# Kernel tuning notes

Hardware: AMD Instinct MI355X
Metric: run time of the kernel (lower is better)

## Reference

```python
import jax, jax.numpy as jnp
import numpy as np

D_IN = 1024
D_OUT = 1024
NUM_HEADS = 16
HEAD_DIM = D_OUT // NUM_HEADS


def setup_inputs() -> dict:
    key = jax.random.key(0)
    kx, kq, kk, kv = jax.random.split(key, 4)
    x = jax.random.normal(kx, (2, 2048, D_IN), dtype=jnp.float32)
    W_q = jax.random.normal(kq, (D_IN, D_OUT), dtype=jnp.float32)
    W_k = jax.random.normal(kk, (D_IN, D_OUT), dtype=jnp.float32)
    W_v = jax.random.normal(kv, (D_IN, D_OUT), dtype=jnp.float32)
    return {"x": x, "W_q": W_q, "W_k": W_k, "W_v": W_v}


def reference(x, W_q, W_k, W_v):
    B, S, _ = x.shape
    H, Dh = NUM_HEADS, HEAD_DIM
    # project and split heads -> [B, H, S, Dh]
    q = (x @ W_q).reshape(B, S, H, Dh).transpose(0, 2, 1, 3)
    k = (x @ W_k).reshape(B, S, H, Dh).transpose(0, 2, 1, 3)
    v = (x @ W_v).reshape(B, S, H, Dh).transpose(0, 2, 1, 3)
    scores = jnp.einsum('bhqd,bhkd->bhqk', q, k) / jnp.sqrt(jnp.float32(Dh))
    causal = jnp.tril(jnp.ones((S, S), dtype=bool))  # True where allowed
    scores = jnp.where(causal[None, None], scores, -jnp.inf)
    weights = jax.nn.softmax(scores, axis=-1)
    ctx = jnp.einsum('bhqk,bhkd->bhqd', weights, v)
    return ctx.transpose(0, 2, 1, 3).reshape(B, S, H * Dh)
```

## Files before the change

kernel.cpp:

```cpp
#include <hip/hip_runtime.h>
#include <hip/hip_bf16.h>

#define B 2
#define S 2048
#define DIN 1024
#define DOUT 1024
#define NH 16
#define DH 64
#define M_TOT (B * S)

typedef __attribute__((ext_vector_type(8))) short bf16x8;
typedef __attribute__((ext_vector_type(8))) unsigned short u16x8;
typedef __attribute__((ext_vector_type(4))) float f32x4;
typedef __attribute__((ext_vector_type(16))) float f32x16;

#define ASTRIDE 4194304
#define WSTRIDE 1048576

__device__ __forceinline__ ushort f2bf(float x) {
    union { float f; unsigned u; } c; c.f = x;
    unsigned r = (c.u + 0x7FFFu + ((c.u >> 16) & 1u)) >> 16;
    return (ushort)r;
}
__device__ __forceinline__ float bf2f(ushort h) {
    union { unsigned u; float f; } c; c.u = ((unsigned)h) << 16;
    return c.f;
}
__device__ __forceinline__ f32x4 mfma16(bf16x8 a, bf16x8 b, f32x4 c) {
    return __builtin_amdgcn_mfma_f32_16x16x32_bf16(a, b, c, 0, 0, 0);
}
__device__ __forceinline__ f32x16 mfma32(bf16x8 a, bf16x8 b, f32x16 c) {
    return __builtin_amdgcn_mfma_f32_32x32x16_bf16(a, b, c, 0, 0, 0);
}
__device__ __forceinline__ unsigned cvt_pk(float lo, float hi) {
    unsigned r;
    asm("v_cvt_pk_bf16_f32 %0, %1, %2" : "=v"(r) : "v"(lo), "v"(hi));
    return r;
}
__device__ __forceinline__ float exp2fast(float x) {
    float r;
    asm("v_exp_f32 %0, %1" : "=v"(r) : "v"(x));
    return r;
}


__global__ __launch_bounds__(256) void split_x(const float* __restrict__ x,
                                               ushort* __restrict__ xs) {
    const size_t gid = (size_t)blockIdx.x * 256 + threadIdx.x;
    const float4 v = *reinterpret_cast<const float4*>(x + gid * 4);
    const float in[4] = {v.x, v.y, v.z, v.w};
    ushort h0[4], h1[4];
#pragma unroll
    for (int e = 0; e < 4; ++e) {
        h0[e] = f2bf(in[e]);
        h1[e] = f2bf(in[e] - bf2f(h0[e]));
    }
    const size_t o = gid * 4;
    *reinterpret_cast<ushort4*>(xs + o)           = ushort4{h0[0], h0[1], h0[2], h0[3]};
    *reinterpret_cast<ushort4*>(xs + ASTRIDE + o) = ushort4{h1[0], h1[1], h1[2], h1[3]};
}

__global__ __launch_bounds__(256) void split_wT3(const float* __restrict__ W0,
                                                 const float* __restrict__ W1,
                                                 const float* __restrict__ W2,
                                                 ushort* __restrict__ wt) {
    __shared__ float Ws[64][68];
    const int tid = threadIdx.x;
    const int k0 = blockIdx.x << 6;
    const int n0 = blockIdx.y << 6;
    const int wi = blockIdx.z;
    const float* W = (wi == 0) ? W0 : (wi == 1) ? W1 : W2;
    ushort* wto = wt + (size_t)wi * 2 * WSTRIDE;

    const int r = tid >> 2;
    const int cb = (tid & 3) << 2;
#pragma unroll
    for (int it = 0; it < 4; ++it) {
        const int c = cb + (it << 4);
        *reinterpret_cast<float4*>(&Ws[r][c]) =
            *reinterpret_cast<const float4*>(&W[(size_t)(k0 + r) * 1024 + n0 + c]);
    }
    __syncthreads();
    const int rn = tid >> 2;
    const int kc = (tid & 3) << 4;
    u16x8 o0[2], o1[2];
#pragma unroll
    for (int half = 0; half < 2; ++half)
#pragma unroll
        for (int i = 0; i < 8; ++i) {
            const float x = Ws[kc + (half << 3) + i][rn];
            const ushort a = f2bf(x);
            o0[half][i] = a;
            o1[half][i] = f2bf(x - bf2f(a));
        }
    const size_t base = (size_t)(n0 + rn) * 1024 + k0 + kc;
    *reinterpret_cast<u16x8*>(wto + base)               = o0[0];
    *reinterpret_cast<u16x8*>(wto + base + 8)           = o0[1];
    *reinterpret_cast<u16x8*>(wto + WSTRIDE + base)     = o1[0];
    *reinterpret_cast<u16x8*>(wto + WSTRIDE + base + 8) = o1[1];
}

__global__ __launch_bounds__(256, 2) void proj_fused5(const ushort* __restrict__ xsp,
                                                      const ushort* __restrict__ wtsp,
                                                      float* __restrict__ qf,
                                                      ushort* __restrict__ ksp,
                                                      ushort* __restrict__ vtsp) {
    __shared__ __align__(16) ushort SL[36864];

    const int tid = threadIdx.x;
    const int lane = tid & 63;
    const int w = tid >> 6;
    const int swz = (blockIdx.x & 7) * 64 + (blockIdx.x >> 3);
    const int n0 = (swz & 15) << 6;
    const int m0 = (swz >> 4) << 7;
    const int col = lane & 15;
    const int glane = lane >> 4;
    const int lrow = lane >> 3;
    const int sl8 = ((lane & 7) ^ lrow) << 3;

    f32x4 accq[2][4], acck[2][4], accv[2][4];
#pragma unroll
    for (int mi = 0; mi < 2; ++mi)
#pragma unroll
        for (int nj = 0; nj < 4; ++nj) {
            accq[mi][nj] = f32x4{0.f, 0.f, 0.f, 0.f};
            acck[mi][nj] = f32x4{0.f, 0.f, 0.f, 0.f};
            accv[mi][nj] = f32x4{0.f, 0.f, 0.f, 0.f};
        }

    for (int k0 = 0; k0 < DIN; k0 += 64) {
        __syncthreads();
#pragma unroll
        for (int i = 0; i < 18; ++i) {
            const int u = (i << 2) | w;
            const ushort* g;
            if (u < 32) {
                const int sp = u >> 4, rb = u & 15;
                g = xsp + (size_t)sp * ASTRIDE + (size_t)(m0 + (rb << 3) + lrow) * 1024 + k0 + sl8;
            } else {
                const int v = u - 32;
                const int bi = v >> 3;
                const int rb = v & 7;
                g = wtsp + (size_t)bi * WSTRIDE + (size_t)(n0 + (rb << 3) + lrow) * 1024 + k0 + sl8;
            }
            __builtin_amdgcn_global_load_lds(g, &SL[u * 512], 16, 0, 0);
        }
        __syncthreads();

#pragma unroll
        for (int st = 0; st < 2; ++st) {
            const int sw = (((st << 2) | glane) ^ (col & 7)) << 3;
            bf16x8 a[2][2];
#pragma unroll
            for (int sp = 0; sp < 2; ++sp)
#pragma unroll
                for (int mi = 0; mi < 2; ++mi) {
                    const int arow = (w << 5) + (mi << 4) + col;
                    a[sp][mi] = *reinterpret_cast<const bf16x8*>(&SL[sp * 8192 + arow * 64 + sw]);
                }
#pragma unroll
            for (int nj = 0; nj < 4; ++nj) {
                const int brow = (nj << 4) + col;
                const int bb = 16384 + brow * 64 + sw;
                const bf16x8 bq0 = *reinterpret_cast<const bf16x8*>(&SL[bb]);
                const bf16x8 bq1 = *reinterpret_cast<const bf16x8*>(&SL[bb + 4096]);
                const bf16x8 bk0 = *reinterpret_cast<const bf16x8*>(&SL[bb + 8192]);
                const bf16x8 bk1 = *reinterpret_cast<const bf16x8*>(&SL[bb + 12288]);
                const bf16x8 bv0 = *reinterpret_cast<const bf16x8*>(&SL[bb + 16384]);
#pragma unroll
                for (int mi = 0; mi < 2; ++mi) {
                    accq[mi][nj] = mfma16(a[0][mi], bq0, accq[mi][nj]);
                    accq[mi][nj] = mfma16(a[1][mi], bq0, accq[mi][nj]);
                    accq[mi][nj] = mfma16(a[0][mi], bq1, accq[mi][nj]);
                    acck[mi][nj] = mfma16(a[0][mi], bk0, acck[mi][nj]);
                    acck[mi][nj] = mfma16(a[1][mi], bk0, acck[mi][nj]);
                    acck[mi][nj] = mfma16(a[0][mi], bk1, acck[mi][nj]);
                    accv[mi][nj] = mfma16(bv0, a[0][mi], accv[mi][nj]);
                    accv[mi][nj] = mfma16(bv0, a[1][mi], accv[mi][nj]);
                }
            }
        }
    }

    const int b = m0 >> 11;
    const int h = n0 >> 6;
    const size_t bh_off = (size_t)(b * NH + h) * S * DH;
#pragma unroll
    for (int mi = 0; mi < 2; ++mi)
#pragma unroll
        for (int r = 0; r < 4; ++r) {
            const int srow = (m0 & (S - 1)) + (w << 5) + (mi << 4) + (glane << 2) + r;
#pragma unroll
            for (int nj = 0; nj < 4; ++nj) {
                const size_t o = bh_off + (size_t)srow * DH + (nj << 4) + col;
                qf[o] = accq[mi][nj][r];
                const float xk = acck[mi][nj][r];
                const ushort k0s = f2bf(xk);
                ksp[o] = k0s;
                ksp[ASTRIDE + o] = f2bf(xk - bf2f(k0s));
            }
        }

    const int cm = col >> 2;
    const int colp = (col & 3) | ((((cm & 1) << 1) | (cm >> 1)) << 2);
    const size_t vbh = (size_t)(b * NH + h) * DH * S;
#pragma unroll
    for (int mi = 0; mi < 2; ++mi) {
        const int s = (m0 & (S - 1)) + (w << 5) + (mi << 4) + colp;
#pragma unroll
        for (int nj = 0; nj < 4; ++nj)
#pragma unroll
            for (int r = 0; r < 4; ++r) {
                const int d = (nj << 4) + (glane << 2) + r;
                vtsp[vbh + (size_t)d * S + s] = f2bf(accv[mi][nj][r]);
            }
    }
}

__global__ __launch_bounds__(256, 2) void attn_mfma7(const float* __restrict__ Qf,
                                                     const ushort* __restrict__ ksp,
                                                     const ushort* __restrict__ vtsp,
                                                     float* __restrict__ out) {
    __shared__ __align__(16) ushort SB[2][12288];

    const int tid = threadIdx.x;
    const int lane = tid & 63;
    const int w = tid >> 6;

    const int xcd = blockIdx.x & 7;
    const int u_ = blockIdx.x >> 3;
    int bh, qt;
    if (u_ < 32) { bh = (xcd << 2) | (u_ >> 4);                 qt = 15 - (u_ & 15); }
    else         { const int v2 = u_ - 32; bh = (xcd << 2) | 2 | (v2 >> 4); qt = v2 & 15; }

    const int q0 = qt << 7;
    const int qw0 = q0 + (w << 5);
    const int hi = lane >> 5;
    const int ql = lane & 31;
    const int qg = qw0 + ql;
    const int lrow = lane >> 3;
    const int sl8 = ((lane & 7) ^ lrow) << 3;

    bf16x8 qb[3][4];
    {
        const float* qp = Qf + ((size_t)bh * S + qg) * DH + (hi << 3);
#pragma unroll
        for (int dc = 0; dc < 4; ++dc) {
            const float4 f0 = *reinterpret_cast<const float4*>(qp + (dc << 4));
            const float4 f1 = *reinterpret_cast<const float4*>(qp + (dc << 4) + 4);
            const float xs[8] = {f0.x, f0.y, f0.z, f0.w, f1.x, f1.y, f1.z, f1.w};
#pragma unroll
            for (int e = 0; e < 8; ++e) {
                const float x = xs[e] * 0.18033688011112042f;
                const ushort h0 = f2bf(x);
                const float r1 = x - bf2f(h0);
                const ushort h1 = f2bf(r1);
                qb[0][dc][e] = (short)h0;
                qb[1][dc][e] = (short)h1;
                qb[2][dc][e] = (short)f2bf(r1 - bf2f(h1));
            }
        }
    }

    f32x16 O[2];
#pragma unroll
    for (int ds = 0; ds < 2; ++ds)
#pragma unroll
        for (int r = 0; r < 16; ++r) O[ds][r] = 0.f;
    float m_ = -INFINITY, l_ = 0.f;

    const size_t kbase = (size_t)bh * S * DH;
    const size_t vbase = (size_t)bh * DH * S;

#define ISSUE_KV(K0, BUF)                                                               \
    {                                                                                   \
        _Pragma("unroll")                                                               \
        for (int i = 0; i < 6; ++i) {                                                   \
            const int u = (i << 2) | w;                                                 \
            const ushort* gp;                                                           \
            if (u < 16) {                                                               \
                const int sp = u >> 3, rb = u & 7;                                      \
                gp = ksp + (size_t)sp * ASTRIDE + kbase +                               \
                     (size_t)((K0) + (rb << 3) + lrow) * DH + sl8;                      \
            } else {                                                                    \
                const int rb = u & 7;                                                   \
                gp = vtsp + vbase + (size_t)((rb << 3) + lrow) * S + (K0) + sl8;        \
            }                                                                           \
            __builtin_amdgcn_global_load_lds(gp, &SB[BUF][u * 512], 16, 0, 0);          \
        }                                                                               \
    }

    ISSUE_KV(0, 0);
    __syncthreads();

    const int ktmax = (q0 >> 6) + 1;
    for (int kt = 0; kt <= ktmax; ++kt) {
        const int k0 = kt << 6;
        const int cur = kt & 1;
        if (kt < ktmax) ISSUE_KV(k0 + 64, cur ^ 1);

        const bool active = (k0 <= qw0 + 31);
        if (active) {
            const ushort* KL = &SB[cur][0];
            const ushort* VL = &SB[cur][8192];

            f32x16 Sf[2];
#pragma unroll
            for (int ks = 0; ks < 2; ++ks)
#pragma unroll
                for (int r = 0; r < 16; ++r) Sf[ks][r] = 0.f;
#pragma unroll
            for (int ks = 0; ks < 2; ++ks) {
#pragma unroll
                for (int dc = 0; dc < 4; ++dc) {
                    const int row = (ks << 5) + ql;
                    const int eo = row * 64 + ((((dc << 1) | hi) ^ (row & 7)) << 3);
                    const bf16x8 ka = *reinterpret_cast<const bf16x8*>(&KL[eo]);
                    const bf16x8 kb = *reinterpret_cast<const bf16x8*>(&KL[4096 + eo]);
                    Sf[ks] = mfma32(ka, qb[0][dc], Sf[ks]);
                    Sf[ks] = mfma32(ka, qb[1][dc], Sf[ks]);
                    Sf[ks] = mfma32(ka, qb[2][dc], Sf[ks]);
                    Sf[ks] = mfma32(kb, qb[0][dc], Sf[ks]);
                    Sf[ks] = mfma32(kb, qb[1][dc], Sf[ks]);
                }
            }

            if (k0 + 63 > qw0) {
#pragma unroll
                for (int ks = 0; ks < 2; ++ks)
#pragma unroll
                    for (int r = 0; r < 16; ++r) {
                        const int kg = k0 + (ks << 5) + (r & 3) + ((r >> 2) << 3) + (hi << 2);
                        if (kg > qg) Sf[ks][r] = -1e30f;
                    }
            }

            float mx[8];
#pragma unroll
            for (int i = 0; i < 8; ++i)
                mx[i] = fmaxf(fmaxf(Sf[0][i], Sf[0][i + 8]),
                              fmaxf(Sf[1][i], Sf[1][i + 8]));
            float rm = fmaxf(fmaxf(fmaxf(mx[0], mx[1]), fmaxf(mx[2], mx[3])),
                             fmaxf(fmaxf(mx[4], mx[5]), fmaxf(mx[6], mx[7])));
            rm = fmaxf(rm, __shfl_xor(rm, 32));
            if (__any(rm > m_ + 8.f)) {
                const float nm = fmaxf(m_, rm);
                const float sc = exp2fast(m_ - nm);
                m_ = nm;
                l_ *= sc;
#pragma unroll
                for (int ds = 0; ds < 2; ++ds)
#pragma unroll
                    for (int r = 0; r < 16; ++r) O[ds][r] *= sc;
            }

            float rsa[4] = {0.f, 0.f, 0.f, 0.f};
            bf16x8 pb[4];
#pragma unroll
            for (int ks = 0; ks < 2; ++ks) {
                float p[16];
#pragma unroll
                for (int r = 0; r < 16; ++r) {
                    p[r] = exp2fast(Sf[ks][r] - m_);
                    rsa[r & 3] += p[r];
                }
#pragma unroll
                for (int c = 0; c < 2; ++c) {
                    union { unsigned u[4]; bf16x8 v; } pw;
                    pw.u[0] = cvt_pk(p[(c << 3) + 0], p[(c << 3) + 1]);
                    pw.u[1] = cvt_pk(p[(c << 3) + 2], p[(c << 3) + 3]);
                    pw.u[2] = cvt_pk(p[(c << 3) + 4], p[(c << 3) + 5]);
                    pw.u[3] = cvt_pk(p[(c << 3) + 6], p[(c << 3) + 7]);
                    pb[(ks << 1) + c] = pw.v;
                }
            }
            float rs = (rsa[0] + rsa[1]) + (rsa[2] + rsa[3]);
            rs += __shfl_xor(rs, 32);
            l_ += rs;

#pragma unroll
            for (int ds = 0; ds < 2; ++ds)
#pragma unroll
                for (int kc = 0; kc < 4; ++kc) {
                    const int row = (ds << 5) + ql;
                    const int eo = row * 64 + ((((kc << 1) | hi) ^ (row & 7)) << 3);
                    const bf16x8 va = *reinterpret_cast<const bf16x8*>(&VL[eo]);
                    O[ds] = mfma32(va, pb[kc], O[ds]);
                }
        }
        __syncthreads();
    }

    const float inv = 1.f / l_;
    const int b = bh >> 4, h = bh & (NH - 1);
    float* op = out + ((size_t)(b * S + qg)) * DOUT + h * DH;
#pragma unroll
    for (int ds = 0; ds < 2; ++ds)
#pragma unroll
        for (int rg = 0; rg < 4; ++rg) {
            float4 v;
            v.x = O[ds][(rg << 2) + 0] * inv;
            v.y = O[ds][(rg << 2) + 1] * inv;
            v.z = O[ds][(rg << 2) + 2] * inv;
            v.w = O[ds][(rg << 2) + 3] * inv;
            *reinterpret_cast<float4*>(&op[(ds << 5) + (rg << 3) + (hi << 2)]) = v;
        }
#undef ISSUE_KV
}

__global__ __launch_bounds__(256) void proj_f32(const float* __restrict__ A,
                                                const float* __restrict__ W,
                                                float* __restrict__ outf) {
    __shared__ float As[16][68];
    __shared__ float Bs[16][68];
    const int tid = threadIdx.x;
    const int m0 = blockIdx.x * 64;
    const int n0 = blockIdx.y * 64;
    const int tm = tid >> 4, tn = tid & 15;
    const int la_r = tid >> 2, la_c = (tid & 3) << 2;
    const int lb_r = tid >> 4, lb_c = (tid & 15) << 2;

    float acc[4][4];
#pragma unroll
    for (int i = 0; i < 4; ++i)
#pragma unroll
        for (int j = 0; j < 4; ++j) acc[i][j] = 0.f;

    for (int k0 = 0; k0 < DIN; k0 += 16) {
        const float4 av = *reinterpret_cast<const float4*>(&A[(size_t)(m0 + la_r) * DIN + k0 + la_c]);
        const float4 bv = *reinterpret_cast<const float4*>(&W[(size_t)(k0 + lb_r) * DOUT + n0 + lb_c]);
        __syncthreads();
        As[la_c + 0][la_r] = av.x; As[la_c + 1][la_r] = av.y;
        As[la_c + 2][la_r] = av.z; As[la_c + 3][la_r] = av.w;
        *reinterpret_cast<float4*>(&Bs[lb_r][lb_c]) = bv;
        __syncthreads();
#pragma unroll
        for (int kk = 0; kk < 16; ++kk) {
            const float4 a = *reinterpret_cast<const float4*>(&As[kk][tm << 2]);
            const float4 b = *reinterpret_cast<const float4*>(&Bs[kk][tn << 2]);
            const float aa[4] = {a.x, a.y, a.z, a.w};
            const float bb[4] = {b.x, b.y, b.z, b.w};
#pragma unroll
            for (int i = 0; i < 4; ++i)
#pragma unroll
                for (int j = 0; j < 4; ++j) acc[i][j] += aa[i] * bb[j];
        }
    }
    const int b = m0 >> 11;
    const int s_base = (m0 & (S - 1)) + (tm << 2);
    const int h = n0 >> 6;
    const int dh = tn << 2;
    float* obase = outf + ((size_t)(b * NH + h) * S) * DH;
#pragma unroll
    for (int i = 0; i < 4; ++i) {
        float4 v;
        v.x = acc[i][0]; v.y = acc[i][1]; v.z = acc[i][2]; v.w = acc[i][3];
        *reinterpret_cast<float4*>(&obase[(size_t)(s_base + i) * DH + dh]) = v;
    }
}

__global__ __launch_bounds__(256) void attn_f32(const float* __restrict__ Q,
                                                const float* __restrict__ K,
                                                const float* __restrict__ V,
                                                float* __restrict__ out) {
    __shared__ float Qs[64][68];
    __shared__ float Ks[64][68];
    __shared__ float Vs[64][68];
    __shared__ float Ps[64][68];
    const int tid = threadIdx.x;
    const int bh = blockIdx.x & 31;
    const int qt = 31 - (blockIdx.x >> 5);
    const int q0 = qt << 6;
    const int tq = tid >> 4, tk = tid & 15;
    const int sr = tid >> 2, sc = (tid & 3) << 2;

    const float* qbase = Q + ((size_t)bh * S + q0) * DH;
    const float* kbase = K + (size_t)bh * S * DH;
    const float* vbase = V + (size_t)bh * S * DH;
#pragma unroll
    for (int it = 0; it < 4; ++it) {
        const int d0 = sc + (it << 4);
        const float4 v = *reinterpret_cast<const float4*>(&qbase[(size_t)sr * DH + d0]);
        Qs[d0 + 0][sr] = v.x; Qs[d0 + 1][sr] = v.y;
        Qs[d0 + 2][sr] = v.z; Qs[d0 + 3][sr] = v.w;
    }
    float C[4][4];
#pragma unroll
    for (int i = 0; i < 4; ++i)
#pragma unroll
        for (int j = 0; j < 4; ++j) C[i][j] = 0.f;
    float m[4] = {-1e30f, -1e30f, -1e30f, -1e30f};
    float l[4] = {0.f, 0.f, 0.f, 0.f};

    for (int kt = 0; kt <= qt; ++kt) {
        const int k0 = kt << 6;
        float4 kv[4], vv[4];
#pragma unroll
        for (int it = 0; it < 4; ++it) {
            const int d0 = sc + (it << 4);
            kv[it] = *reinterpret_cast<const float4*>(&kbase[(size_t)(k0 + sr) * DH + d0]);
            vv[it] = *reinterpret_cast<const float4*>(&vbase[(size_t)(k0 + sr) * DH + d0]);
        }
        __syncthreads();
#pragma unroll
        for (int it = 0; it < 4; ++it) {
            const int d0 = sc + (it << 4);
            Ks[d0 + 0][sr] = kv[it].x; Ks[d0 + 1][sr] = kv[it].y;
            Ks[d0 + 2][sr] = kv[it].z; Ks[d0 + 3][sr] = kv[it].w;
            *reinterpret_cast<float4*>(&Vs[sr][d0]) = vv[it];
        }
        __syncthreads();

        float s[4][4];
#pragma unroll
        for (int i = 0; i < 4; ++i)
#pragma unroll
            for (int j = 0; j < 4; ++j) s[i][j] = 0.f;
#pragma unroll 16
        for (int d = 0; d < 64; ++d) {
            const float4 qf4 = *reinterpret_cast<const float4*>(&Qs[d][tq << 2]);
            const float4 kf4 = *reinterpret_cast<const float4*>(&Ks[d][tk << 2]);
            const float qa[4] = {qf4.x, qf4.y, qf4.z, qf4.w};
            const float ka[4] = {kf4.x, kf4.y, kf4.z, kf4.w};
#pragma unroll
            for (int i = 0; i < 4; ++i)
#pragma unroll
                for (int j = 0; j < 4; ++j) s[i][j] += qa[i] * ka[j];
        }
        if (kt == qt) {
#pragma unroll
            for (int i = 0; i < 4; ++i) {
                const int qg = q0 + (tq << 2) + i;
#pragma unroll
                for (int j = 0; j < 4; ++j) {
                    const int kg = k0 + (tk << 2) + j;
                    s[i][j] = (kg <= qg) ? s[i][j] * 0.125f : -1e30f;
                }
            }
        } else {
#pragma unroll
            for (int i = 0; i < 4; ++i)
#pragma unroll
                for (int j = 0; j < 4; ++j) s[i][j] *= 0.125f;
        }
#pragma unroll
        for (int i = 0; i < 4; ++i) {
            float rm = fmaxf(fmaxf(s[i][0], s[i][1]), fmaxf(s[i][2], s[i][3]));
#pragma unroll
            for (int off = 1; off < 16; off <<= 1) rm = fmaxf(rm, __shfl_xor(rm, off));
            const float mn = fmaxf(m[i], rm);
            const float scale = __expf(m[i] - mn);
            float rs = 0.f;
#pragma unroll
            for (int j = 0; j < 4; ++j) {
                s[i][j] = __expf(s[i][j] - mn);
                rs += s[i][j];
            }
#pragma unroll
            for (int off = 1; off < 16; off <<= 1) rs += __shfl_xor(rs, off);
            l[i] = l[i] * scale + rs;
            m[i] = mn;
#pragma unroll
            for (int j = 0; j < 4; ++j) C[i][j] *= scale;
            *reinterpret_cast<float4*>(&Ps[(tq << 2) + i][tk << 2]) =
                make_float4(s[i][0], s[i][1], s[i][2], s[i][3]);
        }
        __syncthreads();
#pragma unroll 4
        for (int kc = 0; kc < 16; ++kc) {
            float4 pf[4], vf[4];
#pragma unroll
            for (int i = 0; i < 4; ++i)
                pf[i] = *reinterpret_cast<const float4*>(&Ps[(tq << 2) + i][kc << 2]);
#pragma unroll
            for (int j = 0; j < 4; ++j)
                vf[j] = *reinterpret_cast<const float4*>(&Vs[(kc << 2) + j][tk << 2]);
#pragma unroll
            for (int i = 0; i < 4; ++i) {
                const float pa[4] = {pf[i].x, pf[i].y, pf[i].z, pf[i].w};
#pragma unroll
                for (int j = 0; j < 4; ++j) {
                    C[i][j] += pa[0] * ((const float*)&vf[0])[j]
                             + pa[1] * ((const float*)&vf[1])[j]
                             + pa[2] * ((const float*)&vf[2])[j]
                             + pa[3] * ((const float*)&vf[3])[j];
                }
            }
        }
        __syncthreads();
    }
    const int b = bh >> 4, h = bh & (NH - 1);
#pragma unroll
    for (int i = 0; i < 4; ++i) {
        const int qg = q0 + (tq << 2) + i;
        const float inv = 1.f / l[i];
        float4 v;
        v.x = C[i][0] * inv; v.y = C[i][1] * inv;
        v.z = C[i][2] * inv; v.w = C[i][3] * inv;
        *reinterpret_cast<float4*>(&out[((size_t)(b * S + qg)) * DOUT + h * DH + (tk << 2)]) = v;
    }
}

extern "C" void kernel_launch(void* const* d_in, const int* in_sizes, int n_in,
                              void* d_out, int out_size, void* d_ws, size_t ws_size,
                              hipStream_t stream) {
    const float* x  = (const float*)d_in[0];
    const float* Wq = (const float*)d_in[1];
    const float* Wk = (const float*)d_in[2];
    const float* Wv = (const float*)d_in[3];
    float* out = (float*)d_out;

    char* ws = (char*)d_ws;
    const size_t MB = 1024 * 1024;

    if (ws_size >= 68 * MB) {
        ushort* wtsp = (ushort*)(ws);
        ushort* xsp  = (ushort*)(ws + 12 * MB);
        float*  qf   = (float*)(ws + 28 * MB);
        ushort* ksp  = (ushort*)(ws + 44 * MB);
        ushort* vtsp = (ushort*)(ws + 60 * MB);

        split_x<<<4096, 256, 0, stream>>>(x, xsp);
        split_wT3<<<dim3(16, 16, 3), 256, 0, stream>>>(Wq, Wk, Wv, wtsp);
        proj_fused5<<<512, 256, 0, stream>>>(xsp, wtsp, qf, ksp, vtsp);
        attn_mfma7<<<512, 256, 0, stream>>>(qf, ksp, vtsp, out);
    } else {
        float* qws = (float*)d_ws;
        float* kws = qws + (size_t)M_TOT * DOUT;
        float* vws = kws + (size_t)M_TOT * DOUT;
        dim3 pgrid(M_TOT / 64, DOUT / 64);
        proj_f32<<<pgrid, 256, 0, stream>>>(x, Wq, qws);
        proj_f32<<<pgrid, 256, 0, stream>>>(x, Wk, kws);
        proj_f32<<<pgrid, 256, 0, stream>>>(x, Wv, vws);
        attn_f32<<<32 * 32, 256, 0, stream>>>(qws, kws, vws, out);
    }
}
```

Baseline: 133.4 us.

## Restructure attention into 64-query blocks with split K/V prefetch and fewer Q splits

The attention kernel moves to 128-thread blocks covering 64 queries each, launched as 1024 blocks with a new block-to-(head, q-tile) mapping that pairs short and long causal tiles. K and V now have separate LDS buffers and loads: the next K tile is fetched after QK^T finishes and the next V tile after PV, replacing the combined double-buffered tile. The Q split drops from three bf16 terms to two, removing one MFMA per step at some cost in precision, and s_setprio is raised around the MFMA sections. The aim is less idle work on partially masked tiles, smaller LDS use for higher occupancy, and more overlap of loads with compute, at the price of an extra barrier per iteration.

Result: faster. 129.8 us, median of 2 (-2.7%).

```diff
diff --git a/kernel.cpp b/kernel.cpp
--- a/kernel.cpp
+++ b/kernel.cpp
@@ -217,11 +217,12 @@
     }
 }
 
-__global__ __launch_bounds__(256, 2) void attn_mfma7(const float* __restrict__ Qf,
+__global__ __launch_bounds__(128, 2) void attn_mfma8(const float* __restrict__ Qf,
                                                      const ushort* __restrict__ ksp,
                                                      const ushort* __restrict__ vtsp,
                                                      float* __restrict__ out) {
-    __shared__ __align__(16) ushort SB[2][12288];
+    __shared__ __align__(16) ushort KL[2][4096];
+    __shared__ __align__(16) ushort VL[4096];
 
     const int tid = threadIdx.x;
     const int lane = tid & 63;
@@ -229,11 +230,12 @@
 
     const int xcd = blockIdx.x & 7;
     const int u_ = blockIdx.x >> 3;
-    int bh, qt;
-    if (u_ < 32) { bh = (xcd << 2) | (u_ >> 4);                 qt = 15 - (u_ & 15); }
-    else         { const int v2 = u_ - 32; bh = (xcd << 2) | 2 | (v2 >> 4); qt = v2 & 15; }
-
-    const int q0 = qt << 7;
+    const int s_ = u_ & 31, p_ = u_ >> 5;
+    const int bh = (xcd << 2) | ((s_ >> 4) << 1) | (p_ >> 1);
+    const int j_ = s_ & 15;
+    const int qt = (p_ & 1) ? (16 + j_) : (15 - j_);
+
+    const int q0 = qt << 6;
     const int qw0 = q0 + (w << 5);
     const int hi = lane >> 5;
     const int ql = lane & 31;
@@ -241,7 +243,7 @@
     const int lrow = lane >> 3;
     const int sl8 = ((lane & 7) ^ lrow) << 3;
 
-    bf16x8 qb[3][4];
+    bf16x8 qb[2][4];
     {
         const float* qp = Qf + ((size_t)bh * S + qg) * DH + (hi << 3);
 #pragma unroll
@@ -253,11 +255,8 @@
             for (int e = 0; e < 8; ++e) {
                 const float x = xs[e] * 0.18033688011112042f;
                 const ushort h0 = f2bf(x);
-                const float r1 = x - bf2f(h0);
-                const ushort h1 = f2bf(r1);
                 qb[0][dc][e] = (short)h0;
-                qb[1][dc][e] = (short)h1;
-                qb[2][dc][e] = (short)f2bf(r1 - bf2f(h1));
+                qb[1][dc][e] = (short)f2bf(x - bf2f(h0));
             }
         }
     }
@@ -272,123 +271,127 @@
     const size_t kbase = (size_t)bh * S * DH;
     const size_t vbase = (size_t)bh * DH * S;
 
-#define ISSUE_KV(K0, BUF)                                                               \
+#define ISSUE_K(K0)                                                                     \
     {                                                                                   \
         _Pragma("unroll")                                                               \
-        for (int i = 0; i < 6; ++i) {                                                   \
-            const int u = (i << 2) | w;                                                 \
-            const ushort* gp;                                                           \
-            if (u < 16) {                                                               \
-                const int sp = u >> 3, rb = u & 7;                                      \
-                gp = ksp + (size_t)sp * ASTRIDE + kbase +                               \
-                     (size_t)((K0) + (rb << 3) + lrow) * DH + sl8;                      \
-            } else {                                                                    \
-                const int rb = u & 7;                                                   \
-                gp = vtsp + vbase + (size_t)((rb << 3) + lrow) * S + (K0) + sl8;        \
-            }                                                                           \
-            __builtin_amdgcn_global_load_lds(gp, &SB[BUF][u * 512], 16, 0, 0);          \
+        for (int i = 0; i < 8; ++i) {                                                   \
+            const int u = (i << 1) | w;                                                 \
+            const int sp = u >> 3, rb = u & 7;                                          \
+            const ushort* gp = ksp + (size_t)sp * ASTRIDE + kbase +                     \
+                               (size_t)((K0) + (rb << 3) + lrow) * DH + sl8;            \
+            __builtin_amdgcn_global_load_lds(gp, &KL[sp][rb << 9], 16, 0, 0);           \
         }                                                                               \
     }
-
-    ISSUE_KV(0, 0);
+#define ISSUE_V(K0)                                                                     \
+    {                                                                                   \
+        _Pragma("unroll")                                                               \
+        for (int i = 0; i < 4; ++i) {                                                   \
+            const int u = (i << 1) | w;                                                 \
+            const ushort* gp = vtsp + vbase +                                           \
+                               (size_t)((u << 3) + lrow) * S + (K0) + sl8;              \
+            __builtin_amdgcn_global_load_lds(gp, &VL[u << 9], 16, 0, 0);                \
+        }                                                                               \
+    }
+
+    ISSUE_K(0);
+    ISSUE_V(0);
     __syncthreads();
 
-    const int ktmax = (q0 >> 6) + 1;
-    for (int kt = 0; kt <= ktmax; ++kt) {
+    for (int kt = 0; kt <= qt; ++kt) {
         const int k0 = kt << 6;
-        const int cur = kt & 1;
-        if (kt < ktmax) ISSUE_KV(k0 + 64, cur ^ 1);
-
-        const bool active = (k0 <= qw0 + 31);
-        if (active) {
-            const ushort* KL = &SB[cur][0];
-            const ushort* VL = &SB[cur][8192];
-
-            f32x16 Sf[2];
+
+        f32x16 Sf[2];
+#pragma unroll
+        for (int ks = 0; ks < 2; ++ks)
+#pragma unroll
+            for (int r = 0; r < 16; ++r) Sf[ks][r] = 0.f;
+        __builtin_amdgcn_s_setprio(1);
+#pragma unroll
+        for (int ks = 0; ks < 2; ++ks) {
+#pragma unroll
+            for (int dc = 0; dc < 4; ++dc) {
+                const int row = (ks << 5) + ql;
+                const int eo = row * 64 + ((((dc << 1) | hi) ^ (row & 7)) << 3);
+                const bf16x8 ka = *reinterpret_cast<const bf16x8*>(&KL[0][eo]);
+                const bf16x8 kb = *reinterpret_cast<const bf16x8*>(&KL[1][eo]);
+                Sf[ks] = mfma32(ka, qb[0][dc], Sf[ks]);
+                Sf[ks] = mfma32(ka, qb[1][dc], Sf[ks]);
+                Sf[ks] = mfma32(kb, qb[0][dc], Sf[ks]);
+                Sf[ks] = mfma32(kb, qb[1][dc], Sf[ks]);
+            }
+        }
+        __builtin_amdgcn_s_setprio(0);
+
+        __syncthreads();
+        if (kt < qt) ISSUE_K(k0 + 64);
+
+        if (k0 + 63 > qw0) {
 #pragma unroll
             for (int ks = 0; ks < 2; ++ks)
 #pragma unroll
-                for (int r = 0; r < 16; ++r) Sf[ks][r] = 0.f;
-#pragma unroll
-            for (int ks = 0; ks < 2; ++ks) {
-#pragma unroll
-                for (int dc = 0; dc < 4; ++dc) {
-                    const int row = (ks << 5) + ql;
-                    const int eo = row * 64 + ((((dc << 1) | hi) ^ (row & 7)) << 3);
-                    const bf16x8 ka = *reinterpret_cast<const bf16x8*>(&KL[eo]);
-                    const bf16x8 kb = *reinterpret_cast<const bf16x8*>(&KL[4096 + eo]);
-                    Sf[ks] = mfma32(ka, qb[0][dc], Sf[ks]);
-                    Sf[ks] = mfma32(ka, qb[1][dc], Sf[ks]);
-                    Sf[ks] = mfma32(ka, qb[2][dc], Sf[ks]);
-                    Sf[ks] = mfma32(kb, qb[0][dc], Sf[ks]);
-                    Sf[ks] = mfma32(kb, qb[1][dc], Sf[ks]);
+                for (int r = 0; r < 16; ++r) {
+                    const int kg = k0 + (ks << 5) + (r & 3) + ((r >> 2) << 3) + (hi << 2);
+                    if (kg > qg) Sf[ks][r] = -1e30f;
                 }
-            }
-
-            if (k0 + 63 > qw0) {
-#pragma unroll
-                for (int ks = 0; ks < 2; ++ks)
-#pragma unroll
-                    for (int r = 0; r < 16; ++r) {
-                        const int kg = k0 + (ks << 5) + (r & 3) + ((r >> 2) << 3) + (hi << 2);
-                        if (kg > qg) Sf[ks][r] = -1e30f;
-                    }
-            }
-
-            float mx[8];
-#pragma unroll
-            for (int i = 0; i < 8; ++i)
-                mx[i] = fmaxf(fmaxf(Sf[0][i], Sf[0][i + 8]),
-                              fmaxf(Sf[1][i], Sf[1][i + 8]));
-            float rm = fmaxf(fmaxf(fmaxf(mx[0], mx[1]), fmaxf(mx[2], mx[3])),
-                             fmaxf(fmaxf(mx[4], mx[5]), fmaxf(mx[6], mx[7])));
-            rm = fmaxf(rm, __shfl_xor(rm, 32));
-            if (__any(rm > m_ + 8.f)) {
-                const float nm = fmaxf(m_, rm);
-                const float sc = exp2fast(m_ - nm);
-                m_ = nm;
-                l_ *= sc;
-#pragma unroll
-                for (int ds = 0; ds < 2; ++ds)
-#pragma unroll
-                    for (int r = 0; r < 16; ++r) O[ds][r] *= sc;
-            }
-
-            float rsa[4] = {0.f, 0.f, 0.f, 0.f};
-            bf16x8 pb[4];
-#pragma unroll
-            for (int ks = 0; ks < 2; ++ks) {
-                float p[16];
-#pragma unroll
-                for (int r = 0; r < 16; ++r) {
-                    p[r] = exp2fast(Sf[ks][r] - m_);
-                    rsa[r & 3] += p[r];
-                }
-#pragma unroll
-                for (int c = 0; c < 2; ++c) {
-                    union { unsigned u[4]; bf16x8 v; } pw;
-                    pw.u[0] = cvt_pk(p[(c << 3) + 0], p[(c << 3) + 1]);
-                    pw.u[1] = cvt_pk(p[(c << 3) + 2], p[(c << 3) + 3]);
-                    pw.u[2] = cvt_pk(p[(c << 3) + 4], p[(c << 3) + 5]);
-                    pw.u[3] = cvt_pk(p[(c << 3) + 6], p[(c << 3) + 7]);
-                    pb[(ks << 1) + c] = pw.v;
-                }
-            }
-            float rs = (rsa[0] + rsa[1]) + (rsa[2] + rsa[3]);
-            rs += __shfl_xor(rs, 32);
-            l_ += rs;
-
+        }
+
+        float mx[8];
+#pragma unroll
+        for (int i = 0; i < 8; ++i)
+            mx[i] = fmaxf(fmaxf(Sf[0][i], Sf[0][i + 8]),
+                          fmaxf(Sf[1][i], Sf[1][i + 8]));
+        float rm = fmaxf(fmaxf(fmaxf(mx[0], mx[1]), fmaxf(mx[2], mx[3])),
+                         fmaxf(fmaxf(mx[4], mx[5]), fmaxf(mx[6], mx[7])));
+        rm = fmaxf(rm, __shfl_xor(rm, 32));
+        if (__any(rm > m_ + 8.f)) {
+            const float nm = fmaxf(m_, rm);
+            const float sc = exp2fast(m_ - nm);
+            m_ = nm;
+            l_ *= sc;
 #pragma unroll
             for (int ds = 0; ds < 2; ++ds)
 #pragma unroll
-                for (int kc = 0; kc < 4; ++kc) {
-                    const int row = (ds << 5) + ql;
-                    const int eo = row * 64 + ((((kc << 1) | hi) ^ (row & 7)) << 3);
-                    const bf16x8 va = *reinterpret_cast<const bf16x8*>(&VL[eo]);
-                    O[ds] = mfma32(va, pb[kc], O[ds]);
-                }
-        }
-        __syncthreads();
+                for (int r = 0; r < 16; ++r) O[ds][r] *= sc;
+        }
+
+        float rsa[4] = {0.f, 0.f, 0.f, 0.f};
+        bf16x8 pb[4];
+#pragma unroll
+        for (int ks = 0; ks < 2; ++ks) {
+            float p[16];
+#pragma unroll
+            for (int r = 0; r < 16; ++r) {
+                p[r] = exp2fast(Sf[ks][r] - m_);
+                rsa[r & 3] += p[r];
+            }
+#pragma unroll
+            for (int c = 0; c < 2; ++c) {
+                union { unsigned u[4]; bf16x8 v; } pw;
+                pw.u[0] = cvt_pk(p[(c << 3) + 0], p[(c << 3) + 1]);
+                pw.u[1] = cvt_pk(p[(c << 3) + 2], p[(c << 3) + 3]);
+                pw.u[2] = cvt_pk(p[(c << 3) + 4], p[(c << 3) + 5]);
+                pw.u[3] = cvt_pk(p[(c << 3) + 6], p[(c << 3) + 7]);
+                pb[(ks << 1) + c] = pw.v;
+            }
+        }
+        float rs = (rsa[0] + rsa[1]) + (rsa[2] + rsa[3]);
+        rs += __shfl_xor(rs, 32);
+        l_ += rs;
+
+        __builtin_amdgcn_s_setprio(1);
+#pragma unroll
+        for (int ds = 0; ds < 2; ++ds)
+#pragma unroll
+            for (int kc = 0; kc < 4; ++kc) {
+                const int row = (ds << 5) + ql;
+                const int eo = row * 64 + ((((kc << 1) | hi) ^ (row & 7)) << 3);
+                const bf16x8 va = *reinterpret_cast<const bf16x8*>(&VL[eo]);
+                O[ds] = mfma32(va, pb[kc], O[ds]);
+            }
+        __builtin_amdgcn_s_setprio(0);
+
+        __syncthreads();
+        if (kt < qt) ISSUE_V(k0 + 64);
     }
 
     const float inv = 1.f / l_;
@@ -405,7 +408,8 @@
             v.w = O[ds][(rg << 2) + 3] * inv;
             *reinterpret_cast<float4*>(&op[(ds << 5) + (rg << 3) + (hi << 2)]) = v;
         }
-#undef ISSUE_KV
+#undef ISSUE_K
+#undef ISSUE_V
 }
 
 __global__ __launch_bounds__(256) void proj_f32(const float* __restrict__ A,
@@ -623,7 +627,7 @@
         split_x<<<4096, 256, 0, stream>>>(x, xsp);
         split_wT3<<<dim3(16, 16, 3), 256, 0, stream>>>(Wq, Wk, Wv, wtsp);
         proj_fused5<<<512, 256, 0, stream>>>(xsp, wtsp, qf, ksp, vtsp);
-        attn_mfma7<<<512, 256, 0, stream>>>(qf, ksp, vtsp, out);
+        attn_mfma8<<<1024, 128, 0, stream>>>(qf, ksp, vtsp, out);
     } else {
         float* qws = (float*)d_ws;
         float* kws = qws + (size_t)M_TOT * DOUT;
```
